# Performance work log

Hardware: AMD Instinct MI355X
Metric: run time of the kernel (lower is better)

Reference implementation:

```python
import jax, jax.numpy as jnp
import numpy as np

B, D, NH, NT = 4096, 2048, 16, 4
DK = D // NH
EPS = 1e-5


def setup_inputs() -> dict:
    key = jax.random.key(0)
    ks = jax.random.split(key, 16)
    s = 0.02
    inp = {
        "e0": jax.random.normal(ks[0], (B, D), jnp.float32),
        "e1": jax.random.normal(ks[1], (B, D), jnp.float32),
        "e2": jax.random.normal(ks[2], (B, D), jnp.float32),
        "e3": jax.random.normal(ks[3], (B, D), jnp.float32),
        "quality": jax.random.uniform(ks[4], (B, NT), jnp.float32),
        "Wq": jax.random.normal(ks[5], (D, D), jnp.float32) * s,
        "bq": jnp.zeros((D,), jnp.float32),
        "Wk": jax.random.normal(ks[6], (D, D), jnp.float32) * s,
        "bk": jnp.zeros((D,), jnp.float32),
        "Wv": jax.random.normal(ks[7], (D, D), jnp.float32) * s,
        "bv": jnp.zeros((D,), jnp.float32),
        "Wo": jax.random.normal(ks[8], (D, D), jnp.float32) * s,
        "bo": jnp.zeros((D,), jnp.float32),
        "gamma": jnp.ones((D,), jnp.float32),
        "beta": jnp.zeros((D,), jnp.float32),
    }
    return inp


def _layer_norm(x, gamma, beta):
    mu = jnp.mean(x, axis=-1, keepdims=True)
    var = jnp.mean(jnp.square(x - mu), axis=-1, keepdims=True)
    return (x - mu) * jax.lax.rsqrt(var + EPS) * gamma + beta


def reference(e0, e1, e2, e3, quality, Wq, bq, Wk, bk, Wv, bv, Wo, bo, gamma, beta):
    # H: (B, T=4, D) stacked evidence representations
    H = jnp.stack([e0, e1, e2, e3], axis=1)
    # QKV projections, reshaped to (B, heads, T, dk)
    def proj(W, b):
        return (jnp.einsum('btd,ed->bte', H, W) + b).reshape(B, NT, NH, DK).transpose(0, 2, 1, 3)
    Q, K, V = proj(Wq, bq), proj(Wk, bk), proj(Wv, bv)
    # scores: (B, heads, Tq, Tk), scaled then multiplicatively quality-gated on keys
    scores = jnp.einsum('bhid,bhjd->bhij', Q, K) / jnp.sqrt(jnp.float32(DK))
    scores = scores * quality[:, None, None, :]
    attn = jax.nn.softmax(scores, axis=-1)  # dropout = identity at inference
    ctx = jnp.einsum('bhij,bhjd->bhid', attn, V)          # (B, H, T, dk)
    ctx = ctx.transpose(0, 2, 1, 3).reshape(B, NT, D)      # (B, T, D)
    ctx = jnp.einsum('btd,ed->bte', ctx, Wo) + bo
    fused = jnp.mean(ctx, axis=1)       # mean over evidence types
    residual = jnp.mean(H, axis=1)      # mean of ALL evidence types
    return _layer_norm(fused + residual, gamma, beta)
```

## Files before the change

kernel.cpp:

```cpp
#include <hip/hip_runtime.h>
#include <cstdint>
#include <cstddef>

#define BB 4096
#define DD 2048
#define NHH 16
#define NTT 4
#define DKK 128

using u16 = unsigned short;
using u32 = unsigned int;

typedef __bf16 bf16x8 __attribute__((ext_vector_type(8)));
typedef float f32x4 __attribute__((ext_vector_type(4)));

__device__ __forceinline__ float b2f(u16 u) {
    union { float f; u32 i; } c; c.i = ((u32)u) << 16; return c.f;
}
__device__ __forceinline__ u16 f2b(float f) {
    union { float f; u32 i; } c; c.f = f;
    u32 x = c.i;
    u32 r = (x + 0x7fffu + ((x >> 16) & 1u)) >> 16;
    return (u16)r;
}
__device__ __forceinline__ u32 pk(float lo, float hi) {
    u32 a = __builtin_bit_cast(u32, lo) + 0x8000u;
    u32 b = __builtin_bit_cast(u32, hi) + 0x8000u;
    return __builtin_amdgcn_perm(b, a, 0x07060302u);
}

__device__ __forceinline__ void load_lds16(const void* g, void* l) {
    __builtin_amdgcn_global_load_lds((const __attribute__((address_space(1))) void*)g,
                                     (__attribute__((address_space(3))) void*)l,
                                     16, 0, 0);
}

__global__ __launch_bounds__(256) void cvt_all(
    const float* __restrict__ e0, const float* __restrict__ e1,
    const float* __restrict__ e2, const float* __restrict__ e3,
    const float* __restrict__ Wq, const float* __restrict__ Wk,
    const float* __restrict__ Wv, const float* __restrict__ Wo,
    u16* __restrict__ Ebf, u16* __restrict__ W4)
{
    const int blk = blockIdx.x;
    const float* src;
    u16* dst;
    size_t i;
    if (blk < 16384) {
        const int t = blk & 3, b = blk >> 2;
        src = ((t == 0) ? e0 : (t == 1) ? e1 : (t == 2) ? e2 : e3) + (size_t)b * DD;
        dst = Ebf + (size_t)blk * DD;
        i = threadIdx.x * 8;
    } else {
        const int wb = blk - 16384;
        const int w = wb >> 11;
        src = (w == 0) ? Wq : (w == 1) ? Wk : (w == 2) ? Wv : Wo;
        dst = W4 + (size_t)w * DD * DD;
        i = (size_t)(wb & 2047) * 2048 + threadIdx.x * 8;
    }
    float4 a = *(const float4*)(src + i);
    float4 c = *(const float4*)(src + i + 4);
    *(uint4*)(dst + i) = make_uint4(pk(a.x, a.y), pk(a.z, a.w),
                                    pk(c.x, c.y), pk(c.z, c.w));
}

__global__ __launch_bounds__(256, 2) void qkv_attn(
    const u16* __restrict__ Ebf,
    const u16* __restrict__ Wqb, const u16* __restrict__ Wkb,
    const u16* __restrict__ Wvb,
    const float* __restrict__ bq, const float* __restrict__ bk,
    const float* __restrict__ bv, const float* __restrict__ qual,
    u16* __restrict__ ctx)
{
    __shared__ __align__(16) u16 As [128 * 64];
    __shared__ __align__(16) u16 BQs[128 * 64];
    __shared__ __align__(16) u16 BKs[128 * 64];
    __shared__ __align__(16) u16 BVs[128 * 64];

    const int tid = threadIdx.x;
    const int h = blockIdx.x;
    const int m0 = blockIdx.y * 128;
    const int n0 = h * 128;

    const int wave = tid >> 6;
    const int lane = tid & 63;

    const int srow = wave * 8 + (lane >> 3);
    const int scol = ((lane & 7) ^ (lane >> 3)) * 8;
    const u16* srcA = Ebf + (size_t)(m0 + srow) * DD + scol;
    const u16* srcQ = Wqb + (size_t)(n0 + srow) * DD + scol;
    const u16* srcK = Wkb + (size_t)(n0 + srow) * DD + scol;
    const u16* srcV = Wvb + (size_t)(n0 + srow) * DD + scol;

    char* ldsA = (char*)As  + wave * 1024;
    char* ldsQ = (char*)BQs + wave * 1024;
    char* ldsK = (char*)BKs + wave * 1024;
    char* ldsV = (char*)BVs + wave * 1024;

    const int lrow = lane & 15;
    const int q4 = lane >> 4;
    const int wm = wave * 32;
    const int soff0 = (q4 ^ (lrow & 7)) * 16;
    const int aoff0 = (wm + lrow) * 128;
    const int aoff1 = aoff0 + 16 * 128;
    const int boffr = lrow * 128;

    f32x4 aQ[2][8] = {};
    f32x4 aK[2][8] = {};
    f32x4 aV[2][8] = {};

    for (int k0 = 0; k0 < DD; k0 += 64) {
        __syncthreads();
#pragma unroll
        for (int i = 0; i < 4; ++i) {
            const size_t go = (size_t)i * 32 * DD;
            load_lds16(srcA + go, ldsA + i * 4096);
            load_lds16(srcQ + go, ldsQ + i * 4096);
            load_lds16(srcK + go, ldsK + i * 4096);
            load_lds16(srcV + go, ldsV + i * 4096);
        }
        srcA += 64; srcQ += 64; srcK += 64; srcV += 64;
        __syncthreads();

#pragma unroll
        for (int kk = 0; kk < 2; ++kk) {
            const int so = soff0 ^ (kk * 64);
            bf16x8 af0 = *(const bf16x8*)((const char*)As + aoff0 + so);
            bf16x8 af1 = *(const bf16x8*)((const char*)As + aoff1 + so);
#pragma unroll
            for (int ni = 0; ni < 8; ++ni) {
                const int boff = boffr + ni * 16 * 128 + so;
                bf16x8 bqf = *(const bf16x8*)((const char*)BQs + boff);
                bf16x8 bkf = *(const bf16x8*)((const char*)BKs + boff);
                bf16x8 bvf = *(const bf16x8*)((const char*)BVs + boff);
                aQ[0][ni] = __builtin_amdgcn_mfma_f32_16x16x32_bf16(af0, bqf, aQ[0][ni], 0, 0, 0);
                aQ[1][ni] = __builtin_amdgcn_mfma_f32_16x16x32_bf16(af1, bqf, aQ[1][ni], 0, 0, 0);
                aK[0][ni] = __builtin_amdgcn_mfma_f32_16x16x32_bf16(af0, bkf, aK[0][ni], 0, 0, 0);
                aK[1][ni] = __builtin_amdgcn_mfma_f32_16x16x32_bf16(af1, bkf, aK[1][ni], 0, 0, 0);
                aV[0][ni] = __builtin_amdgcn_mfma_f32_16x16x32_bf16(af0, bvf, aV[0][ni], 0, 0, 0);
                aV[1][ni] = __builtin_amdgcn_mfma_f32_16x16x32_bf16(af1, bvf, aV[1][ni], 0, 0, 0);
            }
        }
    }

    const int quad = lane >> 4;
    const int lcol = lane & 15;

    float qb[8], kb[8], vb[8];
#pragma unroll
    for (int ni = 0; ni < 8; ++ni) {
        const int col = n0 + ni * 16 + lcol;
        qb[ni] = bq[col]; kb[ni] = bk[col]; vb[ni] = bv[col];
    }

#pragma unroll
    for (int mi = 0; mi < 2; ++mi) {
        const int bbat = (m0 >> 2) + wave * 8 + mi * 4 + quad;

        float ps[4][4];
#pragma unroll
        for (int t = 0; t < 4; ++t)
#pragma unroll
            for (int j = 0; j < 4; ++j) ps[t][j] = 0.f;

#pragma unroll
        for (int ni = 0; ni < 8; ++ni) {
            float qv[4], kv[4];
#pragma unroll
            for (int t = 0; t < 4; ++t) {
                qv[t] = aQ[mi][ni][t] + qb[ni];
                kv[t] = aK[mi][ni][t] + kb[ni];
            }
#pragma unroll
            for (int t = 0; t < 4; ++t)
#pragma unroll
                for (int j = 0; j < 4; ++j) ps[t][j] += qv[t] * kv[j];
        }
#pragma unroll
        for (int t = 0; t < 4; ++t)
#pragma unroll
            for (int j = 0; j < 4; ++j) {
                ps[t][j] += __shfl_xor(ps[t][j], 1);
                ps[t][j] += __shfl_xor(ps[t][j], 2);
                ps[t][j] += __shfl_xor(ps[t][j], 4);
                ps[t][j] += __shfl_xor(ps[t][j], 8);
            }

        const float scale = 0.08838834764831845f;
        float qj[4];
#pragma unroll
        for (int j = 0; j < 4; ++j) qj[j] = qual[bbat * 4 + j] * scale;

        float wsum[4] = {0.f, 0.f, 0.f, 0.f};
#pragma unroll
        for (int t = 0; t < 4; ++t) {
            float sm[4]; float mx = -1e30f;
#pragma unroll
            for (int j = 0; j < 4; ++j) { sm[j] = ps[t][j] * qj[j]; mx = fmaxf(mx, sm[j]); }
            float ex[4]; float se = 0.f;
#pragma unroll
            for (int j = 0; j < 4; ++j) { ex[j] = __expf(sm[j] - mx); se += ex[j]; }
            const float inv = 0.25f / se;
#pragma unroll
            for (int j = 0; j < 4; ++j) wsum[j] += ex[j] * inv;
        }

#pragma unroll
        for (int ni = 0; ni < 8; ++ni) {
            const int col = n0 + ni * 16 + lcol;
            float r = wsum[0] * aV[mi][ni][0] + wsum[1] * aV[mi][ni][1]
                    + wsum[2] * aV[mi][ni][2] + wsum[3] * aV[mi][ni][3] + vb[ni];
            ctx[(size_t)bbat * DD + col] = f2b(r);
        }
    }
}

__global__ __launch_bounds__(256) void o_gemm(
    const u16* __restrict__ A, const u16* __restrict__ W,
    const float* __restrict__ bia, float* __restrict__ Y)
{
    __shared__ __align__(16) u16 As[128 * 64];
    __shared__ __align__(16) u16 Bs[128 * 64];

    const int tid = threadIdx.x;
    const int m0 = blockIdx.x * 128;
    const int n0 = blockIdx.y * 128;

    const int wave = tid >> 6;
    const int lane = tid & 63;

    const int srow = wave * 8 + (lane >> 3);
    const int scol = ((lane & 7) ^ (lane >> 3)) * 8;
    const u16* srcA = A + (size_t)(m0 + srow) * DD + scol;
    const u16* srcB = W + (size_t)(n0 + srow) * DD + scol;

    char* ldsA = (char*)As + wave * 1024;
    char* ldsB = (char*)Bs + wave * 1024;

    const int wm = (wave >> 1) * 64;
    const int wn = (wave & 1) * 64;
    const int lrow = lane & 15;
    const int q4 = lane >> 4;
    const int soff0 = (q4 ^ (lrow & 7)) * 16;

    f32x4 acc[4][4] = {};

    for (int k0 = 0; k0 < DD; k0 += 64) {
        __syncthreads();
#pragma unroll
        for (int i = 0; i < 4; ++i) {
            const size_t go = (size_t)i * 32 * DD;
            load_lds16(srcA + go, ldsA + i * 4096);
            load_lds16(srcB + go, ldsB + i * 4096);
        }
        srcA += 64; srcB += 64;
        __syncthreads();

#pragma unroll
        for (int kk = 0; kk < 2; ++kk) {
            const int so = soff0 ^ (kk * 64);
            bf16x8 af[4], bfr[4];
#pragma unroll
            for (int i = 0; i < 4; ++i)
                af[i] = *(const bf16x8*)((const char*)As + (wm + i * 16 + lrow) * 128 + so);
#pragma unroll
            for (int i = 0; i < 4; ++i)
                bfr[i] = *(const bf16x8*)((const char*)Bs + (wn + i * 16 + lrow) * 128 + so);
#pragma unroll
            for (int mi = 0; mi < 4; ++mi)
#pragma unroll
                for (int ni = 0; ni < 4; ++ni)
                    acc[mi][ni] = __builtin_amdgcn_mfma_f32_16x16x32_bf16(af[mi], bfr[ni], acc[mi][ni], 0, 0, 0);
        }
    }

#pragma unroll
    for (int mi = 0; mi < 4; ++mi) {
#pragma unroll
        for (int r = 0; r < 4; ++r) {
            const int grow = m0 + wm + mi * 16 + (lane >> 4) * 4 + r;
#pragma unroll
            for (int ni = 0; ni < 4; ++ni) {
                const int gcol = n0 + wn + ni * 16 + (lane & 15);
                Y[(size_t)grow * DD + gcol] = acc[mi][ni][r] + bia[gcol];
            }
        }
    }
}

__global__ __launch_bounds__(256) void ln_kernel(
    const float* __restrict__ Y,
    const float* __restrict__ e0, const float* __restrict__ e1,
    const float* __restrict__ e2, const float* __restrict__ e3,
    const float* __restrict__ gamma, const float* __restrict__ beta,
    float* __restrict__ out)
{
    const int r = blockIdx.x;
    const int tid = threadIdx.x;
    const int c = tid * 8;
    const size_t base = (size_t)r * DD + c;

    float v[8];
    {
        float4 y0 = *(const float4*)(Y + base);
        float4 y1 = *(const float4*)(Y + base + 4);
        float a[8] = {0, 0, 0, 0, 0, 0, 0, 0};
        const float* eps[4] = {e0, e1, e2, e3};
#pragma unroll
        for (int qq = 0; qq < 4; ++qq) {
            float4 p0 = *(const float4*)(eps[qq] + base);
            float4 p1 = *(const float4*)(eps[qq] + base + 4);
            a[0] += p0.x; a[1] += p0.y; a[2] += p0.z; a[3] += p0.w;
            a[4] += p1.x; a[5] += p1.y; a[6] += p1.z; a[7] += p1.w;
        }
        float yv[8] = {y0.x, y0.y, y0.z, y0.w, y1.x, y1.y, y1.z, y1.w};
#pragma unroll
        for (int i = 0; i < 8; ++i) v[i] = yv[i] + 0.25f * a[i];
    }

    float s = 0.f, sq = 0.f;
#pragma unroll
    for (int i = 0; i < 8; ++i) { s += v[i]; sq += v[i] * v[i]; }
#pragma unroll
    for (int off = 32; off >= 1; off >>= 1) {
        s += __shfl_xor(s, off);
        sq += __shfl_xor(sq, off);
    }
    __shared__ float sh[8];
    const int lane = tid & 63, wv = tid >> 6;
    if (lane == 0) { sh[wv] = s; sh[4 + wv] = sq; }
    __syncthreads();
    s = sh[0] + sh[1] + sh[2] + sh[3];
    sq = sh[4] + sh[5] + sh[6] + sh[7];

    const float invD = 1.0f / 2048.0f;
    const float mu = s * invD;
    const float rs = rsqrtf(sq * invD - mu * mu + 1e-5f);

    float4 g0 = *(const float4*)(gamma + c);
    float4 g1 = *(const float4*)(gamma + c + 4);
    float4 b0 = *(const float4*)(beta + c);
    float4 b1 = *(const float4*)(beta + c + 4);
    float gg[8] = {g0.x, g0.y, g0.z, g0.w, g1.x, g1.y, g1.z, g1.w};
    float bb[8] = {b0.x, b0.y, b0.z, b0.w, b1.x, b1.y, b1.z, b1.w};

    float o[8];
#pragma unroll
    for (int i = 0; i < 8; ++i) o[i] = (v[i] - mu) * rs * gg[i] + bb[i];
    *(float4*)(out + base)     = make_float4(o[0], o[1], o[2], o[3]);
    *(float4*)(out + base + 4) = make_float4(o[4], o[5], o[6], o[7]);
}

extern "C" void kernel_launch(void* const* d_in, const int* in_sizes, int n_in,
                              void* d_out, int out_size, void* d_ws, size_t ws_size,
                              hipStream_t stream)
{
    const float* e0   = (const float*)d_in[0];
    const float* e1   = (const float*)d_in[1];
    const float* e2   = (const float*)d_in[2];
    const float* e3   = (const float*)d_in[3];
    const float* qual = (const float*)d_in[4];
    const float* Wq   = (const float*)d_in[5];
    const float* bq   = (const float*)d_in[6];
    const float* Wk   = (const float*)d_in[7];
    const float* bk   = (const float*)d_in[8];
    const float* Wv   = (const float*)d_in[9];
    const float* bv   = (const float*)d_in[10];
    const float* Wo   = (const float*)d_in[11];
    const float* bo   = (const float*)d_in[12];
    const float* gm   = (const float*)d_in[13];
    const float* bt   = (const float*)d_in[14];

    const size_t WD = (size_t)DD * DD;
    const size_t MQ = (size_t)BB * NTT * DD;
    const size_t ED = (size_t)BB * DD;

    u16* Ebf = (u16*)d_ws;
    u16* W4  = Ebf + MQ;
    u16* ctx = W4 + 4 * WD;
    float* Y = (float*)(ctx + ED);

    cvt_all<<<dim3(24576), 256, 0, stream>>>(e0, e1, e2, e3, Wq, Wk, Wv, Wo,
                                             Ebf, W4);

    qkv_attn<<<dim3(16, 128), 256, 0, stream>>>(Ebf, W4, W4 + WD, W4 + 2 * WD,
                                                bq, bk, bv, qual, ctx);

    o_gemm<<<dim3(32, 16), 256, 0, stream>>>(ctx, W4 + 3 * WD, bo, Y);

    ln_kernel<<<dim3(4096), 256, 0, stream>>>(Y, e0, e1, e2, e3, gm, bt,
                                              (float*)d_out);
}
```

Measured before the change: 641.8 us.

## Split QKV-attention wave tiling into a 2x2 grid with cross-wave score exchange

Changes the per-wave tile in the fused QKV+attention kernel from 32 rows by 128 columns to 64 rows by 64 columns (a 2x2 wave grid). This balances A and B fragment LDS reads per MFMA (4 A plus 12 B loads feed 48 MFMAs, instead of 2 A plus 24 B for 48), cutting LDS read traffic. Because each wave now covers only half the head dimension, partial QK dot products are written to a new shared buffer and summed with the partner wave after an extra barrier before the softmax. The cost is one extra LDS exchange and a sync in the epilogue.

New measurement: 723.9 us. 12.8% more time.

```diff
diff --git a/kernel.cpp b/kernel.cpp
--- a/kernel.cpp
+++ b/kernel.cpp
@@ -76,6 +76,7 @@
     __shared__ __align__(16) u16 BQs[128 * 64];
     __shared__ __align__(16) u16 BKs[128 * 64];
     __shared__ __align__(16) u16 BVs[128 * 64];
+    __shared__ float exch[4][4][4][16];
 
     const int tid = threadIdx.x;
     const int h = blockIdx.x;
@@ -99,15 +100,13 @@
 
     const int lrow = lane & 15;
     const int q4 = lane >> 4;
-    const int wm = wave * 32;
+    const int wm = (wave >> 1) * 64;
+    const int wn = (wave & 1) * 64;
     const int soff0 = (q4 ^ (lrow & 7)) * 16;
-    const int aoff0 = (wm + lrow) * 128;
-    const int aoff1 = aoff0 + 16 * 128;
-    const int boffr = lrow * 128;
-
-    f32x4 aQ[2][8] = {};
-    f32x4 aK[2][8] = {};
-    f32x4 aV[2][8] = {};
+
+    f32x4 aQ[4][4] = {};
+    f32x4 aK[4][4] = {};
+    f32x4 aV[4][4] = {};
 
     for (int k0 = 0; k0 < DD; k0 += 64) {
         __syncthreads();
@@ -125,38 +124,41 @@
 #pragma unroll
         for (int kk = 0; kk < 2; ++kk) {
             const int so = soff0 ^ (kk * 64);
-            bf16x8 af0 = *(const bf16x8*)((const char*)As + aoff0 + so);
-            bf16x8 af1 = *(const bf16x8*)((const char*)As + aoff1 + so);
-#pragma unroll
-            for (int ni = 0; ni < 8; ++ni) {
-                const int boff = boffr + ni * 16 * 128 + so;
-                bf16x8 bqf = *(const bf16x8*)((const char*)BQs + boff);
-                bf16x8 bkf = *(const bf16x8*)((const char*)BKs + boff);
-                bf16x8 bvf = *(const bf16x8*)((const char*)BVs + boff);
-                aQ[0][ni] = __builtin_amdgcn_mfma_f32_16x16x32_bf16(af0, bqf, aQ[0][ni], 0, 0, 0);
-                aQ[1][ni] = __builtin_amdgcn_mfma_f32_16x16x32_bf16(af1, bqf, aQ[1][ni], 0, 0, 0);
-                aK[0][ni] = __builtin_amdgcn_mfma_f32_16x16x32_bf16(af0, bkf, aK[0][ni], 0, 0, 0);
-                aK[1][ni] = __builtin_amdgcn_mfma_f32_16x16x32_bf16(af1, bkf, aK[1][ni], 0, 0, 0);
-                aV[0][ni] = __builtin_amdgcn_mfma_f32_16x16x32_bf16(af0, bvf, aV[0][ni], 0, 0, 0);
-                aV[1][ni] = __builtin_amdgcn_mfma_f32_16x16x32_bf16(af1, bvf, aV[1][ni], 0, 0, 0);
+            bf16x8 af[4];
+#pragma unroll
+            for (int mi = 0; mi < 4; ++mi)
+                af[mi] = *(const bf16x8*)((const char*)As + (wm + mi * 16 + lrow) * 128 + so);
+            bf16x8 bq4[4], bk4[4], bv4[4];
+#pragma unroll
+            for (int ni = 0; ni < 4; ++ni) {
+                const int boff = (wn + ni * 16 + lrow) * 128 + so;
+                bq4[ni] = *(const bf16x8*)((const char*)BQs + boff);
+                bk4[ni] = *(const bf16x8*)((const char*)BKs + boff);
+                bv4[ni] = *(const bf16x8*)((const char*)BVs + boff);
             }
+#pragma unroll
+            for (int mi = 0; mi < 4; ++mi)
+#pragma unroll
+                for (int ni = 0; ni < 4; ++ni) {
+                    aQ[mi][ni] = __builtin_amdgcn_mfma_f32_16x16x32_bf16(af[mi], bq4[ni], aQ[mi][ni], 0, 0, 0);
+                    aK[mi][ni] = __builtin_amdgcn_mfma_f32_16x16x32_bf16(af[mi], bk4[ni], aK[mi][ni], 0, 0, 0);
+                    aV[mi][ni] = __builtin_amdgcn_mfma_f32_16x16x32_bf16(af[mi], bv4[ni], aV[mi][ni], 0, 0, 0);
+                }
         }
     }
 
     const int quad = lane >> 4;
     const int lcol = lane & 15;
 
-    float qb[8], kb[8], vb[8];
-#pragma unroll
-    for (int ni = 0; ni < 8; ++ni) {
-        const int col = n0 + ni * 16 + lcol;
+    float qb[4], kb[4], vb[4];
+#pragma unroll
+    for (int ni = 0; ni < 4; ++ni) {
+        const int col = n0 + wn + ni * 16 + lcol;
         qb[ni] = bq[col]; kb[ni] = bk[col]; vb[ni] = bv[col];
     }
 
 #pragma unroll
-    for (int mi = 0; mi < 2; ++mi) {
-        const int bbat = (m0 >> 2) + wave * 8 + mi * 4 + quad;
-
+    for (int mi = 0; mi < 4; ++mi) {
         float ps[4][4];
 #pragma unroll
         for (int t = 0; t < 4; ++t)
@@ -164,7 +166,7 @@
             for (int j = 0; j < 4; ++j) ps[t][j] = 0.f;
 
 #pragma unroll
-        for (int ni = 0; ni < 8; ++ni) {
+        for (int ni = 0; ni < 4; ++ni) {
             float qv[4], kv[4];
 #pragma unroll
             for (int t = 0; t < 4; ++t) {
@@ -185,8 +187,26 @@
                 ps[t][j] += __shfl_xor(ps[t][j], 4);
                 ps[t][j] += __shfl_xor(ps[t][j], 8);
             }
-
-        const float scale = 0.08838834764831845f;
+        if (lcol == 0) {
+#pragma unroll
+            for (int t = 0; t < 4; ++t)
+#pragma unroll
+                for (int j = 0; j < 4; ++j)
+                    exch[wave][mi][quad][t * 4 + j] = ps[t][j];
+        }
+    }
+    __syncthreads();
+
+    const float scale = 0.08838834764831845f;
+#pragma unroll
+    for (int mi = 0; mi < 4; ++mi) {
+        const int bbat = (m0 >> 2) + (wave >> 1) * 16 + mi * 4 + quad;
+
+        float s16[16];
+#pragma unroll
+        for (int v = 0; v < 16; ++v)
+            s16[v] = exch[wave][mi][quad][v] + exch[wave ^ 1][mi][quad][v];
+
         float qj[4];
 #pragma unroll
         for (int j = 0; j < 4; ++j) qj[j] = qual[bbat * 4 + j] * scale;
@@ -196,7 +216,7 @@
         for (int t = 0; t < 4; ++t) {
             float sm[4]; float mx = -1e30f;
 #pragma unroll
-            for (int j = 0; j < 4; ++j) { sm[j] = ps[t][j] * qj[j]; mx = fmaxf(mx, sm[j]); }
+            for (int j = 0; j < 4; ++j) { sm[j] = s16[t * 4 + j] * qj[j]; mx = fmaxf(mx, sm[j]); }
             float ex[4]; float se = 0.f;
 #pragma unroll
             for (int j = 0; j < 4; ++j) { ex[j] = __expf(sm[j] - mx); se += ex[j]; }
@@ -206,8 +226,8 @@
         }
 
 #pragma unroll
-        for (int ni = 0; ni < 8; ++ni) {
-            const int col = n0 + ni * 16 + lcol;
+        for (int ni = 0; ni < 4; ++ni) {
+            const int col = n0 + wn + ni * 16 + lcol;
             float r = wsum[0] * aV[mi][ni][0] + wsum[1] * aV[mi][ni][1]
                     + wsum[2] * aV[mi][ni][2] + wsum[3] * aV[mi][ni][3] + vb[ni];
             ctx[(size_t)bbat * DD + col] = f2b(r);
```
